# Performance work log

Hardware: AMD Instinct MI355X
Metric: run time of the kernel (lower is better)

## Reference

```python
import jax, jax.numpy as jnp
import numpy as np

EPS = 1e-8

def _cosine(a, b):
    # a: (b,h,s,d), b: (b,1,1,d) -> (b,h,s). torch eps semantics: clamp each norm.
    num = jnp.sum(a * b, axis=-1)
    na = jnp.maximum(jnp.linalg.norm(a, axis=-1), EPS)
    nb = jnp.maximum(jnp.linalg.norm(b, axis=-1), EPS)
    return num / (na * nb)

def setup_inputs() -> dict:
    B, H, S, DH, DM = 2, 16, 2048, 64, 1024
    key = jax.random.key(0)
    ks = jax.random.split(key, 8)
    queries = jax.random.normal(ks[0], (B, H, S, DH), dtype=jnp.float32)
    keys = jax.random.normal(ks[1], (B, H, S, DH), dtype=jnp.float32)
    context = jax.random.normal(ks[2], (B, DM), dtype=jnp.float32)
    prev_state = jax.random.normal(ks[3], (B, S, DH), dtype=jnp.float32)
    # causal mask (1 = keep, 0 = masked), shape (B,1,S,S)
    attention_mask = jnp.broadcast_to(jnp.tril(jnp.ones((S, S), dtype=jnp.int32)), (B, 1, S, S))
    # learned params (Linear weights stored torch-style as (out, in))
    cfm_ctx_w = jax.random.normal(ks[4], (DH, DM), dtype=jnp.float32) / np.sqrt(DM)
    cfm_state_w = jax.random.normal(ks[5], (DH, DH), dtype=jnp.float32) / np.sqrt(DH)
    afm_ctx_w = jax.random.normal(ks[6], (DH, DM), dtype=jnp.float32) / np.sqrt(DM)
    cfm_scale = jnp.full((1,), 0.1, dtype=jnp.float32)
    afm_scale = jnp.full((1,), 0.1, dtype=jnp.float32)
    alpha = jnp.asarray(0.1, dtype=jnp.float32)
    beta = jnp.asarray(0.1, dtype=jnp.float32)
    return dict(queries=queries, keys=keys, context=context, prev_state=prev_state,
                attention_mask=attention_mask, cfm_ctx_w=cfm_ctx_w, cfm_state_w=cfm_state_w,
                cfm_scale=cfm_scale, afm_ctx_w=afm_ctx_w, afm_scale=afm_scale,
                alpha=alpha, beta=beta)

def reference(queries, keys, context, prev_state, attention_mask,
              cfm_ctx_w, cfm_state_w, cfm_scale, afm_ctx_w, afm_scale, alpha, beta):
    B, H, S, DH = queries.shape
    # QK^T / sqrt(d_k): (b,h,s,s)
    attn_scores = jnp.einsum('bhqd,bhkd->bhqk', queries, keys) / jnp.sqrt(jnp.asarray(DH, queries.dtype))
    # ---- CFM ----
    cfm_ctx = (context @ cfm_ctx_w.T)[:, None, None, :]            # (b,1,1,dh)
    witt = _cosine(keys, cfm_ctx)                                   # (b,h,s)
    state = (prev_state @ cfm_state_w.T)[:, None, :, :]             # (b,1,s,dh)
    hamming = jnp.mean(((keys > 0) != (state > 0)).astype(keys.dtype), axis=-1)  # (b,h,s)
    cfm = ((witt + (1.0 - hamming)) * cfm_scale[0])[:, :, None, :]  # (b,h,1,s)
    # ---- AFM (no key_probs -> uniform entropy 1/S) ----
    afm_ctx = (context @ afm_ctx_w.T)[:, None, None, :]
    contradiction = jax.nn.relu(-_cosine(keys, afm_ctx))            # (b,h,s)
    entropy = jnp.full_like(contradiction, 1.0 / S)
    afm = ((contradiction + entropy) * afm_scale[0])[:, :, None, :]
    composite = attn_scores + alpha * cfm - beta * afm
    composite = jnp.where(attention_mask == 0, -jnp.inf, composite)
    return composite
```

## Files before the change

kernel.cpp:

```cpp
#include <hip/hip_runtime.h>
#include <math.h>

#define BB 2
#define HH 16
#define SS 2048
#define DHD 64
#define DMD 1024
#define EPSF 1e-8f
#define NEG_FILL -1.0e30f

typedef __attribute__((ext_vector_type(8))) short bf16x8;
typedef __attribute__((ext_vector_type(4))) float f32x4;

#define WS_BIAS_F   1024
#define WS_CONV_F   66560
#define CONV_ELEMS  (BB * HH * SS * DHD)
#define GRAN_TOTAL  (CONV_ELEMS / 8)
#define WS_NEEDED_B ((size_t)WS_CONV_F * 4 + (size_t)CONV_ELEMS * 2 * 2)

static __device__ __forceinline__ unsigned short f2bf(float f) {
    unsigned u = __float_as_uint(f);
    u += 0x7FFFu + ((u >> 16) & 1u);
    return (unsigned short)(u >> 16);
}
static __device__ __forceinline__ float bf2f(unsigned short h) {
    return __uint_as_float(((unsigned)h) << 16);
}
static __device__ __forceinline__ void cvt8s(const float* p, float scale,
                                             bf16x8& h8, bf16x8& l8) {
    float4 v0 = *(const float4*)p;
    float4 v1 = *(const float4*)(p + 4);
    float vf[8] = {v0.x, v0.y, v0.z, v0.w, v1.x, v1.y, v1.z, v1.w};
    #pragma unroll
    for (int j = 0; j < 8; ++j) {
        float f = vf[j] * scale;
        unsigned short h = f2bf(f);
        h8[j] = (short)h;
        l8[j] = (short)f2bf(f - bf2f(h));
    }
}

__global__ void ctx_kernel(const float* __restrict__ context,
                           const float* __restrict__ cfm_ctx_w,
                           const float* __restrict__ afm_ctx_w,
                           float* __restrict__ ws) {
    int t = threadIdx.x;
    int b = t >> 7, sel = (t >> 6) & 1, o = t & 63;
    const float* W = sel ? afm_ctx_w : cfm_ctx_w;
    const float4* wrow = (const float4*)(W + o * DMD);
    const float4* crow = (const float4*)(context + b * DMD);
    float acc = 0.f;
    for (int m = 0; m < DMD / 4; ++m) {
        float4 w4 = wrow[m];
        float4 c4 = crow[m];
        acc += w4.x * c4.x + w4.y * c4.y + w4.z * c4.z + w4.w * c4.w;
    }
    ws[b * 128 + sel * 64 + o] = acc;
    float sq = acc * acc;
    for (int off = 32; off >= 1; off >>= 1) sq += __shfl_xor(sq, off);
    if (o == 0) ws[256 + b * 2 + sel] = fmaxf(sqrtf(sq), EPSF);
}

__global__ void bias_kernel(const float* __restrict__ keys,
                            const float* __restrict__ prev_state,
                            const float* __restrict__ cfm_state_w,
                            const float* __restrict__ cfm_scale,
                            const float* __restrict__ afm_scale,
                            const float* __restrict__ alpha_p,
                            const float* __restrict__ beta_p,
                            const float* __restrict__ ws_ctx,
                            float* __restrict__ bias_out) {
    int gid = blockIdx.x * 4 + (threadIdx.x >> 6);
    int b = gid >> 11, s = gid & (SS - 1);
    int l = threadIdx.x & 63;
    const float4* prow = (const float4*)(prev_state + ((size_t)b * SS + s) * DHD);
    const float4* wrow = (const float4*)(cfm_state_w + l * DHD);
    float st = 0.f;
    #pragma unroll
    for (int j = 0; j < DHD / 4; ++j) {
        float4 p4 = prow[j], w4 = wrow[j];
        st += p4.x * w4.x + p4.y * w4.y + p4.z * w4.z + p4.w * w4.w;
    }
    unsigned long long smask = __ballot(st > 0.f);

    int h = l >> 2, q = l & 3, d0 = q * 16;
    int sb = (int)((smask >> d0) & 0xFFFFull);
    const float* krow = keys + (((size_t)(b * HH + h)) * SS + s) * DHD + d0;
    const float* cc = ws_ctx + b * 128 + d0;
    const float* ac = ws_ctx + b * 128 + 64 + d0;
    float v0 = 0.f, v1 = 0.f, v2 = 0.f, mism = 0.f;
    #pragma unroll
    for (int j4 = 0; j4 < 4; ++j4) {
        float4 k4 = *(const float4*)(krow + j4 * 4);
        float4 c4 = *(const float4*)(cc + j4 * 4);
        float4 a4 = *(const float4*)(ac + j4 * 4);
        float kf[4] = {k4.x, k4.y, k4.z, k4.w};
        float cf[4] = {c4.x, c4.y, c4.z, c4.w};
        float af[4] = {a4.x, a4.y, a4.z, a4.w};
        #pragma unroll
        for (int j = 0; j < 4; ++j) {
            float kd = kf[j];
            v0 = fmaf(kd, cf[j], v0);
            v1 = fmaf(kd, af[j], v1);
            v2 = fmaf(kd, kd, v2);
            int bit = (sb >> (j4 * 4 + j)) & 1;
            mism += ((kd > 0.f) != (bit != 0)) ? 1.f : 0.f;
        }
    }
    v0 += __shfl_xor(v0, 1); v0 += __shfl_xor(v0, 2);
    v1 += __shfl_xor(v1, 1); v1 += __shfl_xor(v1, 2);
    v2 += __shfl_xor(v2, 1); v2 += __shfl_xor(v2, 2);
    mism += __shfl_xor(mism, 1); mism += __shfl_xor(mism, 2);
    if (q == 0) {
        float nb_c = ws_ctx[256 + b * 2];
        float nb_a = ws_ctx[256 + b * 2 + 1];
        float al = alpha_p[0] * cfm_scale[0];
        float be = beta_p[0] * afm_scale[0];
        float nk = fmaxf(sqrtf(v2), EPSF);
        float witt = v0 / (nk * nb_c);
        float contra = fmaxf(-(v1 / (nk * nb_a)), 0.f);
        float ham = mism * (1.f / 64.f);
        bias_out[(size_t)(b * HH + h) * SS + s] =
            al * (witt + 1.f - ham) - be * (contra + 1.f / (float)SS);
    }
}

__global__ void conv_kernel(const float* __restrict__ K,
                            unsigned short* __restrict__ wsc) {
    unsigned short* hi = wsc;
    unsigned short* lo = wsc + CONV_ELEMS;
    int gid = blockIdx.x * 256 + threadIdx.x;
    int bh = gid >> 14;
    int rem = gid & 16383;
    int u = rem >> 7, r2 = rem & 127;
    int s = r2 >> 6, r3 = r2 & 63;
    int lg = r3 >> 4, lr = r3 & 15;
    size_t sidx = ((size_t)bh * SS + u * 16 + lr) * DHD + s * 32 + lg * 8;
    bf16x8 h8, l8;
    cvt8s(K + sidx, 1.f, h8, l8);
    *(bf16x8*)(hi + (size_t)gid * 8) = h8;
    *(bf16x8*)(lo + (size_t)gid * 8) = l8;
}

#define MFMA16(A, B, C) __builtin_amdgcn_mfma_f32_16x16x32_bf16(A, B, C, 0, 0, 0)

__global__ __launch_bounds__(256, 2) void band_pc(
    const float* __restrict__ Qf,
    const unsigned short* __restrict__ wsc,
    const float* __restrict__ bias, float* __restrict__ out) {
    int L = blockIdx.x;
    int xcd = L & 7, sL = L >> 3;
    int j = sL & 31;
    int bh = ((sL >> 5) << 3) | xcd;
    int tid = threadIdx.x;
    int w = tid >> 6, l = tid & 63, lr = l & 15, lg = l >> 4;
    int lg4 = lg * 4;

    int chunksA = (j >> 1) + 1;
    int chunksA4 = (chunksA + 3) & ~3;
    int chunksZ = 32 - (j >> 1);
    int chunksZ4 = (chunksZ + 3) & ~3;
    if (chunksZ4 > 32) chunksZ4 = 32;
    int nchunks = chunksZ4;
    int ngroups = nchunks >> 2;
    int mygroupsA = chunksA4 >> 2;
    int fillA = chunksA4 * 64;
    int fillZ = chunksZ4 * 64;
    int rowA = j * 32, rowZ = (63 - j) * 32;
    int fr0 = 4 * (ngroups - mygroupsA);
    if (fr0 > 32) fr0 = 32;

    __shared__ unsigned short KB[2][8192];
    __shared__ float BIASL[2048];
    __shared__ float TR[2][16 * 256];

    const unsigned short* Kh = wsc;
    const unsigned short* Kl = wsc + CONV_ELEMS;
    const float* bias_g = bias + (size_t)bh * SS;
    float* ob = out + (size_t)bh * SS * SS;
    size_t kbase = (size_t)bh * 131072;
    f32x4 fneg = {NEG_FILL, NEG_FILL, NEG_FILL, NEG_FILL};

#define LOADCH(cidx, R) do {                                                 \
    _Pragma("unroll")                                                        \
    for (int gi = 0; gi < 8; ++gi) {                                         \
        int g = pw * 8 + gi, u = g >> 2, q = g & 3;                          \
        const unsigned short* src = (q < 2 ? Kh : Kl) + kbase                \
            + (size_t)((cidx) * 4 + u) * 1024 + (q & 1) * 512 + l * 8;       \
        R[gi] = *(const bf16x8*)src;                                         \
    }                                                                        \
} while (0)

#define WRITECH(R, nb) do {                                                  \
    _Pragma("unroll")                                                        \
    for (int gi = 0; gi < 8; ++gi) {                                         \
        int g = pw * 8 + gi, u = g >> 2, q = g & 3;                          \
        *(bf16x8*)&KB[nb][u * 2048 + q * 512 + l * 8] = R[gi];               \
    }                                                                        \
} while (0)

    if (w >= 2) {
        int pw = w - 2;
        #pragma unroll
        for (int i = 0; i < 4; ++i) {
            f32x4 bv = *(const f32x4*)(bias_g + pw * 1024 + i * 256 + l * 4);
            *(f32x4*)&BIASL[pw * 1024 + i * 256 + l * 4] = bv;
        }
        bf16x8 rE[8], rO[8];
        LOADCH(0, rE);
        LOADCH(1, rO);
        WRITECH(rE, 0);
        asm volatile("s_waitcnt lgkmcnt(0)" ::: "memory");
        __builtin_amdgcn_sched_barrier(0);
        for (int c = 0; c < nchunks; c += 2) {
            __builtin_amdgcn_s_barrier();
            if (c + 1 < nchunks) WRITECH(rO, 1);
            if (c + 2 < nchunks) LOADCH(c + 2, rE);
            asm volatile("s_waitcnt lgkmcnt(0)" ::: "memory");
            __builtin_amdgcn_sched_barrier(0);
            __builtin_amdgcn_s_barrier();
            if (c + 2 < nchunks) WRITECH(rE, 0);
            if (c + 3 < nchunks) LOADCH(c + 3, rO);
            asm volatile("s_waitcnt lgkmcnt(0)" ::: "memory");
            __builtin_amdgcn_sched_barrier(0);
        }
    } else {
        int row0 = (w == 0) ? rowA : rowZ;
        int mygroups = (w == 0) ? mygroupsA : ngroups;
        float* trw = &TR[w][0];
        int fr = 0;
        bf16x8 q0h0, q0h1, q0l0, q0l1, q1h0, q1h1, q1l0, q1l1;
        {
            const float* qp = Qf + ((size_t)bh * SS + row0 + lr) * DHD + lg * 8;
            cvt8s(qp, 0.125f, q0h0, q0l0);
            cvt8s(qp + 32, 0.125f, q0h1, q0l1);
            cvt8s(qp + (size_t)16 * DHD, 0.125f, q1h0, q1l0);
            cvt8s(qp + (size_t)16 * DHD + 32, 0.125f, q1h1, q1l1);
        }
        f32x4 acc0[16], acc1[16];
        for (int g = 0; g < ngroups; ++g) {
            if (g < mygroups) {
                #pragma unroll
                for (int cc = 0; cc < 4; ++cc) {
                    __builtin_amdgcn_s_barrier();
                    const unsigned short* kb = &KB[cc & 1][0];
                    #pragma unroll
                    for (int u = 0; u < 4; ++u) {
                        int ui = cc * 4 + u;
                        int ug = g * 16 + ui;
                        bf16x8 kh0 = *(const bf16x8*)&kb[u * 2048 + l * 8];
                        bf16x8 kh1 = *(const bf16x8*)&kb[u * 2048 + 512 + l * 8];
                        bf16x8 kl0 = *(const bf16x8*)&kb[u * 2048 + 1024 + l * 8];
                        bf16x8 kl1 = *(const bf16x8*)&kb[u * 2048 + 1536 + l * 8];
                        f32x4 bv = *(const f32x4*)&BIASL[ug * 16 + lg4];
                        int c0 = ug * 16 + lg4;
                        {
                            int row = row0 + lr;
                            f32x4 a = {0.f, 0.f, 0.f, 0.f};
                            a = MFMA16(kh0, q0h0, a);
                            a = MFMA16(kh1, q0h1, a);
                            a = MFMA16(kh0, q0l0, a);
                            a = MFMA16(kh1, q0l1, a);
                            a = MFMA16(kl0, q0h0, a);
                            a = MFMA16(kl1, q0h1, a);
                            #pragma unroll
                            for (int e = 0; e < 4; ++e) {
                                float x = a[e] + bv[e];
                                if (c0 + e > row) x = NEG_FILL;
                                a[e] = x;
                            }
                            acc0[ui] = a;
                        }
                        {
                            int row = row0 + 16 + lr;
                            f32x4 a = {0.f, 0.f, 0.f, 0.f};
                            a = MFMA16(kh0, q1h0, a);
                            a = MFMA16(kh1, q1h1, a);
                            a = MFMA16(kh0, q1l0, a);
                            a = MFMA16(kh1, q1l1, a);
                            a = MFMA16(kl0, q1h0, a);
                            a = MFMA16(kl1, q1h1, a);
                            #pragma unroll
                            for (int e = 0; e < 4; ++e) {
                                float x = a[e] + bv[e];
                                if (c0 + e > row) x = NEG_FILL;
                                a[e] = x;
                            }
                            acc1[ui] = a;
                        }
                    }
                }
                #pragma unroll
                for (int u16 = 0; u16 < 16; ++u16)
                    *(f32x4*)&trw[lr * 256 + ((u16 * 16 + lg4) ^ ((lr & 7) << 2))] = acc0[u16];
                asm volatile("s_waitcnt lgkmcnt(0)" ::: "memory");
                __builtin_amdgcn_sched_barrier(0);
                #pragma unroll
                for (int r = 0; r < 16; ++r) {
                    f32x4 v = *(const f32x4*)&trw[r * 256 + ((l * 4) ^ ((r & 7) << 2))];
                    __builtin_nontemporal_store(v,
                        (f32x4*)(ob + (size_t)(row0 + r) * SS + g * 256 + l * 4));
                }
                #pragma unroll
                for (int u16 = 0; u16 < 16; ++u16)
                    *(f32x4*)&trw[lr * 256 + ((u16 * 16 + lg4) ^ ((lr & 7) << 2))] = acc1[u16];
                asm volatile("s_waitcnt lgkmcnt(0)" ::: "memory");
                __builtin_amdgcn_sched_barrier(0);
                #pragma unroll
                for (int r = 0; r < 16; ++r) {
                    f32x4 v = *(const f32x4*)&trw[r * 256 + ((l * 4) ^ ((r & 7) << 2))];
                    __builtin_nontemporal_store(v,
                        (f32x4*)(ob + (size_t)(row0 + 16 + r) * SS + g * 256 + l * 4));
                }
            } else {
                #pragma unroll
                for (int cc = 0; cc < 4; ++cc) {
                    __builtin_amdgcn_s_barrier();
                    if (fr < 32) {
                        float* orow = ob + (size_t)(rowA + fr) * SS;
                        for (int c = fillA + l * 4; c < SS; c += 256)
                            __builtin_nontemporal_store(fneg, (f32x4*)(orow + c));
                        ++fr;
                    }
                }
            }
        }
    }

    {
        int remA = 32 - fr0;
        int nZ = (fillZ < SS) ? 32 : 0;
        int total = remA + nZ;
        for (int i = w; i < total; i += 4) {
            int row, f0;
            if (i < remA) { row = rowA + fr0 + i; f0 = fillA; }
            else          { row = rowZ + (i - remA); f0 = fillZ; }
            float* orow = ob + (size_t)row * SS;
            for (int c = f0 + l * 4; c < SS; c += 256)
                __builtin_nontemporal_store(fneg, (f32x4*)(orow + c));
        }
    }
#undef LOADCH
#undef WRITECH
}

#define LOADB(S, unit) do {                                                  \
    size_t _r = ((size_t)bh * SS + (unit) * 16 + lr) * DHD + lg * 8;         \
    cvt8s(K + _r, 1.f, S##h0, S##l0);                                        \
    cvt8s(K + _r + 32, 1.f, S##h1, S##l1);                                   \
    S##bv = *(const f32x4*)(bias_row + (unit) * 16 + lg4);                   \
} while (0)

#define COMP(S, unit) do {                                                   \
    int _c0 = (unit) * 16 + lg4;                                             \
    {                                                                        \
        int _row = row0 + lr;                                                \
        f32x4 _a = {0.f, 0.f, 0.f, 0.f};                                     \
        _a = MFMA16(S##h0, q0h0, _a);                                        \
        _a = MFMA16(S##h1, q0h1, _a);                                        \
        _a = MFMA16(S##h0, q0l0, _a);                                        \
        _a = MFMA16(S##h1, q0l1, _a);                                        \
        _a = MFMA16(S##l0, q0h0, _a);                                        \
        _a = MFMA16(S##l1, q0h1, _a);                                        \
        f32x4 _v;                                                            \
        _Pragma("unroll")                                                    \
        for (int _e = 0; _e < 4; ++_e) {                                     \
            float _x = _a[_e] + S##bv[_e];                                   \
            if (_c0 + _e > _row) _x = NEG_FILL;                              \
            _v[_e] = _x;                                                     \
        }                                                                    \
        __builtin_nontemporal_store(_v, (f32x4*)(ob + (size_t)_row * SS + _c0)); \
    }                                                                        \
    {                                                                        \
        int _row = row0 + 16 + lr;                                           \
        f32x4 _a = {0.f, 0.f, 0.f, 0.f};                                     \
        _a = MFMA16(S##h0, q1h0, _a);                                        \
        _a = MFMA16(S##h1, q1h1, _a);                                        \
        _a = MFMA16(S##h0, q1l0, _a);                                        \
        _a = MFMA16(S##h1, q1l1, _a);                                        \
        _a = MFMA16(S##l0, q1h0, _a);                                        \
        _a = MFMA16(S##l1, q1h1, _a);                                        \
        f32x4 _v;                                                            \
        _Pragma("unroll")                                                    \
        for (int _e = 0; _e < 4; ++_e) {                                     \
            float _x = _a[_e] + S##bv[_e];                                   \
            if (_c0 + _e > _row) _x = NEG_FILL;                              \
            _v[_e] = _x;                                                     \
        }                                                                    \
        __builtin_nontemporal_store(_v, (f32x4*)(ob + (size_t)_row * SS + _c0)); \
    }                                                                        \
} while (0)

__global__ __launch_bounds__(128, 2) void band_fallback(
    const float* __restrict__ Q, const float* __restrict__ K,
    const float* __restrict__ bias, float* __restrict__ out) {
    int L = blockIdx.x;
    int xcd = L & 7, sL = L >> 3;
    int j = sL & 31;
    int bh = ((sL >> 5) << 3) | xcd;
    int tid = threadIdx.x;
    int w = tid >> 6, l = tid & 63, lr = l & 15, lg = l >> 4;
    int lg4 = lg * 4;
    int band = w ? (63 - j) : j;
    int row0 = band * 32;
    int nunits = 2 * band + 2;

    const float* bias_row = bias + (size_t)bh * SS;
    float* ob = out + (size_t)bh * SS * SS;

    bf16x8 q0h0, q0h1, q0l0, q0l1, q1h0, q1h1, q1l0, q1l1;
    {
        const float* qp = Q + ((size_t)bh * SS + row0 + lr) * DHD + lg * 8;
        cvt8s(qp, 0.125f, q0h0, q0l0);
        cvt8s(qp + 32, 0.125f, q0h1, q0l1);
        cvt8s(qp + (size_t)16 * DHD, 0.125f, q1h0, q1l0);
        cvt8s(qp + (size_t)16 * DHD + 32, 0.125f, q1h1, q1l1);
    }

    bf16x8 Ah0, Ah1, Al0, Al1, Bh0, Bh1, Bl0, Bl1;
    f32x4 Abv, Bbv;
    LOADB(A, 0);
    LOADB(B, 1);
    for (int u = 0; u < nunits; u += 2) {
        COMP(A, u);
        if (u + 2 < nunits) LOADB(A, u + 2);
        COMP(B, u + 1);
        if (u + 3 < nunits) LOADB(B, u + 3);
    }

    f32x4 f4 = {NEG_FILL, NEG_FILL, NEG_FILL, NEG_FILL};
    int fill0 = nunits * 16;
    for (int r = 0; r < 32; ++r) {
        float* orow = ob + (size_t)(row0 + r) * SS;
        for (int c = fill0 + l * 4; c < SS; c += 256)
            __builtin_nontemporal_store(f4, (f32x4*)(orow + c));
    }
}

extern "C" void kernel_launch(void* const* d_in, const int* in_sizes, int n_in,
                              void* d_out, int out_size, void* d_ws, size_t ws_size,
                              hipStream_t stream) {
    const float* queries     = (const float*)d_in[0];
    const float* keys        = (const float*)d_in[1];
    const float* context     = (const float*)d_in[2];
    const float* prev_state  = (const float*)d_in[3];
    const float* cfm_ctx_w   = (const float*)d_in[5];
    const float* cfm_state_w = (const float*)d_in[6];
    const float* cfm_scale   = (const float*)d_in[7];
    const float* afm_ctx_w   = (const float*)d_in[8];
    const float* afm_scale   = (const float*)d_in[9];
    const float* alpha_p     = (const float*)d_in[10];
    const float* beta_p      = (const float*)d_in[11];
    float* out = (float*)d_out;
    float* ws  = (float*)d_ws;
    float* bias = ws + WS_BIAS_F;
    unsigned short* wsc = (unsigned short*)(ws + WS_CONV_F);

    ctx_kernel<<<1, 256, 0, stream>>>(context, cfm_ctx_w, afm_ctx_w, ws);
    bias_kernel<<<BB * SS / 4, 256, 0, stream>>>(keys, prev_state, cfm_state_w,
                                                 cfm_scale, afm_scale, alpha_p,
                                                 beta_p, ws, bias);
    if (ws_size >= WS_NEEDED_B) {
        conv_kernel<<<GRAN_TOTAL / 256, 256, 0, stream>>>(keys, wsc);
        band_pc<<<1024, 256, 0, stream>>>(queries, wsc, bias, out);
    } else {
        band_fallback<<<1024, 128, 0, stream>>>(queries, keys, bias, out);
    }
}
```

Before: 192.3 us.

## Shrink LDS footprint to fit three blocks per CU

Replaces the full per-row bias staging in shared memory with a double-buffered 256-entry bias slice that the loader wave refills one group ahead inside its K pipeline. The per-wave transpose buffer is halved by emitting each 16-row accumulator tile in two 8-row passes. Launch bounds are raised from 2 to 3 blocks per CU to exploit the smaller LDS use. The aim is higher occupancy to hide store and load latency, at the cost of tighter register limits (possible spills), extra waitcnt/sync points, and a bias-refill timing dependency on the barrier schedule.

```diff
diff --git a/kernel.cpp b/kernel.cpp
--- a/kernel.cpp
+++ b/kernel.cpp
@@ -144,7 +144,7 @@
 
 #define MFMA16(A, B, C) __builtin_amdgcn_mfma_f32_16x16x32_bf16(A, B, C, 0, 0, 0)
 
-__global__ __launch_bounds__(256, 2) void band_pc(
+__global__ __launch_bounds__(256, 3) void band_pc(
     const float* __restrict__ Qf,
     const unsigned short* __restrict__ wsc,
     const float* __restrict__ bias, float* __restrict__ out) {
@@ -171,8 +171,8 @@
     if (fr0 > 32) fr0 = 32;
 
     __shared__ unsigned short KB[2][8192];
-    __shared__ float BIASL[2048];
-    __shared__ float TR[2][16 * 256];
+    __shared__ float BIASG[2][256];
+    __shared__ float TR[2][8 * 256];
 
     const unsigned short* Kh = wsc;
     const unsigned short* Kl = wsc + CONV_ELEMS;
@@ -201,11 +201,8 @@
 
     if (w >= 2) {
         int pw = w - 2;
-        #pragma unroll
-        for (int i = 0; i < 4; ++i) {
-            f32x4 bv = *(const f32x4*)(bias_g + pw * 1024 + i * 256 + l * 4);
-            *(f32x4*)&BIASL[pw * 1024 + i * 256 + l * 4] = bv;
-        }
+        if (pw == 0)
+            *(f32x4*)&BIASG[0][l * 4] = *(const f32x4*)(bias_g + l * 4);
         bf16x8 rE[8], rO[8];
         LOADCH(0, rE);
         LOADCH(1, rO);
@@ -216,11 +213,23 @@
             __builtin_amdgcn_s_barrier();
             if (c + 1 < nchunks) WRITECH(rO, 1);
             if (c + 2 < nchunks) LOADCH(c + 2, rE);
+            if (pw == 0 && (c & 3) == 2) {
+                int gg = (c >> 2) + 1;
+                if (gg < ngroups)
+                    *(f32x4*)&BIASG[gg & 1][l * 4] =
+                        *(const f32x4*)(bias_g + gg * 256 + l * 4);
+            }
             asm volatile("s_waitcnt lgkmcnt(0)" ::: "memory");
             __builtin_amdgcn_sched_barrier(0);
             __builtin_amdgcn_s_barrier();
             if (c + 2 < nchunks) WRITECH(rE, 0);
             if (c + 3 < nchunks) LOADCH(c + 3, rO);
+            if (pw == 0 && ((c + 1) & 3) == 2) {
+                int gg = ((c + 1) >> 2) + 1;
+                if (gg < ngroups)
+                    *(f32x4*)&BIASG[gg & 1][l * 4] =
+                        *(const f32x4*)(bias_g + gg * 256 + l * 4);
+            }
             asm volatile("s_waitcnt lgkmcnt(0)" ::: "memory");
             __builtin_amdgcn_sched_barrier(0);
         }
@@ -252,7 +261,7 @@
                         bf16x8 kh1 = *(const bf16x8*)&kb[u * 2048 + 512 + l * 8];
                         bf16x8 kl0 = *(const bf16x8*)&kb[u * 2048 + 1024 + l * 8];
                         bf16x8 kl1 = *(const bf16x8*)&kb[u * 2048 + 1536 + l * 8];
-                        f32x4 bv = *(const f32x4*)&BIASL[ug * 16 + lg4];
+                        f32x4 bv = *(const f32x4*)&BIASG[g & 1][ui * 16 + lg4];
                         int c0 = ug * 16 + lg4;
                         {
                             int row = row0 + lr;
@@ -291,26 +300,26 @@
                     }
                 }
                 #pragma unroll
-                for (int u16 = 0; u16 < 16; ++u16)
-                    *(f32x4*)&trw[lr * 256 + ((u16 * 16 + lg4) ^ ((lr & 7) << 2))] = acc0[u16];
-                asm volatile("s_waitcnt lgkmcnt(0)" ::: "memory");
-                __builtin_amdgcn_sched_barrier(0);
-                #pragma unroll
-                for (int r = 0; r < 16; ++r) {
-                    f32x4 v = *(const f32x4*)&trw[r * 256 + ((l * 4) ^ ((r & 7) << 2))];
-                    __builtin_nontemporal_store(v,
-                        (f32x4*)(ob + (size_t)(row0 + r) * SS + g * 256 + l * 4));
-                }
-                #pragma unroll
-                for (int u16 = 0; u16 < 16; ++u16)
-                    *(f32x4*)&trw[lr * 256 + ((u16 * 16 + lg4) ^ ((lr & 7) << 2))] = acc1[u16];
-                asm volatile("s_waitcnt lgkmcnt(0)" ::: "memory");
-                __builtin_amdgcn_sched_barrier(0);
-                #pragma unroll
-                for (int r = 0; r < 16; ++r) {
-                    f32x4 v = *(const f32x4*)&trw[r * 256 + ((l * 4) ^ ((r & 7) << 2))];
-                    __builtin_nontemporal_store(v,
-                        (f32x4*)(ob + (size_t)(row0 + 16 + r) * SS + g * 256 + l * 4));
+                for (int p = 0; p < 4; ++p) {
+                    int half = p & 1;
+                    if ((lr >> 3) == half) {
+                        #pragma unroll
+                        for (int u16 = 0; u16 < 16; ++u16)
+                            *(f32x4*)&trw[(lr & 7) * 256 +
+                                ((u16 * 16 + lg4) ^ ((lr & 7) << 2))]
+                                = (p < 2 ? acc0[u16] : acc1[u16]);
+                    }
+                    asm volatile("s_waitcnt lgkmcnt(0)" ::: "memory");
+                    __builtin_amdgcn_sched_barrier(0);
+                    int rbase = row0 + (p >> 1) * 16 + half * 8;
+                    #pragma unroll
+                    for (int r = 0; r < 8; ++r) {
+                        f32x4 v = *(const f32x4*)&trw[r * 256 + ((l * 4) ^ (r << 2))];
+                        __builtin_nontemporal_store(v,
+                            (f32x4*)(ob + (size_t)(rbase + r) * SS + g * 256 + l * 4));
+                    }
+                    asm volatile("s_waitcnt lgkmcnt(0)" ::: "memory");
+                    __builtin_amdgcn_sched_barrier(0);
                 }
             } else {
                 #pragma unroll
```

New measurement: 433.3 us. 2.25x slower.
